# Performance work log

Measured on AMD Instinct MI355X. Metric: run time of the kernel, lower is better.

The kernel has to match this reference:

```python
import jax, jax.numpy as jnp
import numpy as np

N = 8192
F_IN = 128
OC1 = 64
OC2 = 64
N_CLASS = 16
AVG_DEG = 32.0


def setup_inputs() -> dict:
    key = jax.random.key(0)
    ks = jax.random.split(key, 10)
    # sparse-ish 0/1 adjacency with guaranteed self-loops (every row nonempty)
    A = (jax.random.uniform(ks[0], (N, N)) < (AVG_DEG / N)).astype(jnp.float32)
    A = jnp.maximum(A, jnp.eye(N, dtype=jnp.float32))
    deg = jnp.sum(A, axis=1)                      # [N]
    D = jnp.diag(deg)                             # diagonal degree matrix [N,N]
    X = jax.random.normal(ks[1], (N, F_IN), dtype=jnp.float32)
    s = 0.05
    W1 = jax.random.normal(ks[2], (F_IN, OC1), dtype=jnp.float32) * s
    b1 = jax.random.normal(ks[3], (OC1,), dtype=jnp.float32) * s
    W2 = jax.random.normal(ks[4], (OC1, OC2), dtype=jnp.float32) * s
    b2 = jax.random.normal(ks[5], (OC2,), dtype=jnp.float32) * s
    W3 = jax.random.normal(ks[6], (OC2, N_CLASS), dtype=jnp.float32) * s
    b3 = jax.random.normal(ks[7], (N_CLASS,), dtype=jnp.float32) * s
    return {"D": D, "X": X, "A": A, "W1": W1, "b1": b1,
            "W2": W2, "b2": b2, "W3": W3, "b3": b3}


def reference(D, X, A, W1, b1, W2, b2, W3, b3):
    # per-node degree: max over each row of the diagonal degree matrix
    deg = jnp.max(D, axis=1)                      # [N]
    # dj[0] in the original = degree of the FIRST (lowest-index) neighbor of i
    first_idx = jnp.argmax(A > 0, axis=1)         # [N]
    deg_first = deg[first_idx]                    # [N]
    # w[i,j] = A[i,j] / sqrt(deg_first[i] * deg[j]); zero where A[i,j]==0
    W = A / jnp.sqrt(deg_first[:, None] * deg[None, :])  # [N,N]

    def conv(H, Wl, bl):
        agg = W @ H                               # normalized neighbor aggregation
        return jax.nn.leaky_relu(agg @ Wl + bl)   # Linear + LeakyReLU(0.01)

    H = conv(X, W1, b1)
    # F.dropout in eval mode = identity
    H = conv(H, W2, b2)
    logits = H @ W3 + b3                          # [N, class_num]
    return jax.nn.log_softmax(logits, axis=1)
```

## Files before the change

kernel.cpp:

```cpp
#include <hip/hip_runtime.h>

#define NN   8192
#define FIN  128
#define CAP  128

typedef unsigned int u32x4 __attribute__((ext_vector_type(4)));

__global__ __launch_bounds__(256) void k_scan(
        const float* __restrict__ A,
        int* __restrict__ deg,
        int* __restrict__ first,
        unsigned short* __restrict__ cols,
        float* __restrict__ rsd) {
    __shared__ int s_cols[CAP];
    __shared__ int s_cnt, s_min;

    const int row = blockIdx.x;
    const int t   = threadIdx.x;
    if (t == 0) { s_cnt = 0; s_min = 0x7fffffff; }
    __syncthreads();

    const u32x4* Arow = (const u32x4*)(A + (size_t)row * NN);
    int lmin = 0x7fffffff;
#pragma unroll
    for (int v = 0; v < 8; ++v) {
        const int chunk = t + 256 * v;
        u32x4 q = __builtin_nontemporal_load(Arow + chunk);
        if (q.x | q.y | q.z | q.w) {
            unsigned int w[4] = {q.x, q.y, q.z, q.w};
#pragma unroll
            for (int h = 0; h < 4; ++h) {
                if (w[h]) {
                    int c = chunk * 4 + h;
                    int p = atomicAdd(&s_cnt, 1);
                    if (p < CAP) s_cols[p] = c;
                    lmin = min(lmin, c);
                }
            }
        }
    }
    if (lmin != 0x7fffffff) atomicMin(&s_min, lmin);
    __syncthreads();

    const int n = min(s_cnt, CAP);
    if (t < n) cols[row * CAP + t] = (unsigned short)s_cols[t];
    if (t == 0) {
        deg[row]   = s_cnt;
        first[row] = s_min;
        rsd[row]   = 1.0f / sqrtf((float)s_cnt);
    }
}

__global__ __launch_bounds__(128) void k_agg1(
        const float* __restrict__ X,
        const float* __restrict__ rsd,
        const float* __restrict__ W1,
        const float* __restrict__ b1,
        const int* __restrict__ deg,
        const int* __restrict__ first,
        const unsigned short* __restrict__ cols,
        float* __restrict__ H1) {
    __shared__ unsigned short s_cols[CAP];
    __shared__ float s_rsd[CAP];
    __shared__ float s_part[4][FIN];
    __shared__ float s_agg[FIN];
    __shared__ float s_lin[2][64];

    const int row = blockIdx.x;
    const int t   = threadIdx.x;
    const int n   = min(deg[row], CAP);

    if (t < n) {
        int c = cols[row * CAP + t];
        s_cols[t] = (unsigned short)c;
        s_rsd[t]  = rsd[c];
    }
    __syncthreads();

    {
        const int g = t >> 5, q = t & 31;
        const float4* X4 = (const float4*)X;
        float4 acc = make_float4(0.f, 0.f, 0.f, 0.f);
        for (int k = g; k < n; k += 4) {
            const float4 x = X4[(size_t)s_cols[k] * 32 + q];
            const float  r = s_rsd[k];
            acc.x += r * x.x; acc.y += r * x.y; acc.z += r * x.z; acc.w += r * x.w;
        }
        ((float4*)s_part[g])[q] = acc;
    }
    __syncthreads();

    const float alpha = rsd[first[row]];
    s_agg[t] = alpha * (s_part[0][t] + s_part[1][t] + s_part[2][t] + s_part[3][t]);
    __syncthreads();

    {
        const int c = t & 63, h = t >> 6;
        const int f0 = h * 64;
        float acc = h ? 0.f : b1[c];
#pragma unroll 8
        for (int f = 0; f < 64; ++f)
            acc += s_agg[f0 + f] * W1[(f0 + f) * 64 + c];
        s_lin[h][c] = acc;
    }
    __syncthreads();
    if (t < 64) {
        float a = s_lin[0][t] + s_lin[1][t];
        H1[(size_t)row * 64 + t] = a > 0.f ? a : 0.01f * a;
    }
}

__global__ __launch_bounds__(128) void k_agg2(
        const float* __restrict__ H1,
        const float* __restrict__ rsd,
        const float* __restrict__ W2,
        const float* __restrict__ b2,
        const float* __restrict__ W3,
        const float* __restrict__ b3,
        const int* __restrict__ deg,
        const int* __restrict__ first,
        const unsigned short* __restrict__ cols,
        float* __restrict__ out) {
    __shared__ unsigned short s_cols[CAP];
    __shared__ float s_rsd[CAP];
    __shared__ float s_part[8][64];
    __shared__ float s_agg[64];
    __shared__ float s_lin[2][64];
    __shared__ float s_h2[64];
    __shared__ float s_logit[16];

    const int row = blockIdx.x;
    const int t   = threadIdx.x;
    const int n   = min(deg[row], CAP);

    if (t < n) {
        int c = cols[row * CAP + t];
        s_cols[t] = (unsigned short)c;
        s_rsd[t]  = rsd[c];
    }
    __syncthreads();

    {
        const int g = t >> 4, q = t & 15;
        const float4* H4 = (const float4*)H1;
        float4 acc = make_float4(0.f, 0.f, 0.f, 0.f);
        for (int k = g; k < n; k += 8) {
            const float4 x = H4[(size_t)s_cols[k] * 16 + q];
            const float  r = s_rsd[k];
            acc.x += r * x.x; acc.y += r * x.y; acc.z += r * x.z; acc.w += r * x.w;
        }
        ((float4*)s_part[g])[q] = acc;
    }
    __syncthreads();

    const float alpha = rsd[first[row]];
    if (t < 64) {
        float s = 0.f;
#pragma unroll
        for (int g = 0; g < 8; ++g) s += s_part[g][t];
        s_agg[t] = alpha * s;
    }
    __syncthreads();

    {
        const int c = t & 63, h = t >> 6;
        const int f0 = h * 32;
        float acc = h ? 0.f : b2[c];
#pragma unroll
        for (int f = 0; f < 32; ++f)
            acc += s_agg[f0 + f] * W2[(f0 + f) * 64 + c];
        s_lin[h][c] = acc;
    }
    __syncthreads();
    if (t < 64) {
        float a = s_lin[0][t] + s_lin[1][t];
        s_h2[t] = a > 0.f ? a : 0.01f * a;
    }
    __syncthreads();

    if (t < 64) {
        const int c = t & 15, h = t >> 4;
        const int f0 = h * 16;
        float acc = h ? 0.f : b3[c];
#pragma unroll
        for (int f = 0; f < 16; ++f)
            acc += s_h2[f0 + f] * W3[(f0 + f) * 16 + c];
        s_part[h][c] = acc;
    }
    __syncthreads();
    if (t < 16)
        s_logit[t] = s_part[0][t] + s_part[1][t] + s_part[2][t] + s_part[3][t];
    __syncthreads();

    if (t < 16) {
        float m = -1e30f;
#pragma unroll
        for (int k = 0; k < 16; ++k) m = fmaxf(m, s_logit[k]);
        float s = 0.f;
#pragma unroll
        for (int k = 0; k < 16; ++k) s += expf(s_logit[k] - m);
        out[row * 16 + t] = s_logit[t] - m - logf(s);
    }
}

extern "C" void kernel_launch(void* const* d_in, const int* in_sizes, int n_in,
                              void* d_out, int out_size, void* d_ws, size_t ws_size,
                              hipStream_t stream) {
    const float* X  = (const float*)d_in[1];
    const float* A  = (const float*)d_in[2];
    const float* W1 = (const float*)d_in[3];
    const float* b1 = (const float*)d_in[4];
    const float* W2 = (const float*)d_in[5];
    const float* b2 = (const float*)d_in[6];
    const float* W3 = (const float*)d_in[7];
    const float* b3 = (const float*)d_in[8];

    char* ws = (char*)d_ws;
    float*          rsd   = (float*)(ws);
    int*            deg   = (int*)  (ws + 32768);
    int*            first = (int*)  (ws + 65536);
    float*          H1    = (float*)(ws + 98304);
    unsigned short* cols  = (unsigned short*)(ws + 98304 + 2097152);

    k_scan<<<NN, 256, 0, stream>>>(A, deg, first, cols, rsd);
    k_agg1<<<NN, 128, 0, stream>>>(X, rsd, W1, b1, deg, first, cols, H1);
    k_agg2<<<NN, 128, 0, stream>>>(H1, rsd, W2, b2, W3, b3, deg, first, cols,
                                   (float*)d_out);
}
```

Baseline: 479.8 us.

## Fuse scan and two aggregation stages into one persistent kernel with grid barriers

Replaces three launches with a single persistent kernel of 512 blocks, each owning 16 rows. Neighbor column lists stay in shared memory across phases, and global atomic grid barriers separate the phases. The aim is to cut launch overhead and the global round-trip of the cols/deg/first arrays. The gather loops are also unrolled by two for more memory-level parallelism. The cost is that the A scan, which dominates at 256MB read, now runs on only 512 blocks, which may reduce the bandwidth it achieves. The spin barrier also relies on all blocks being co-resident.

```diff
diff --git a/kernel.cpp b/kernel.cpp
--- a/kernel.cpp
+++ b/kernel.cpp
@@ -1,205 +1,229 @@
 #include <hip/hip_runtime.h>
 
-#define NN   8192
-#define FIN  128
-#define CAP  128
+#define NN    8192
+#define FIN   128
+#define CAP   128
+#define NBLK  512
+#define TPB   256
+#define RPB   16
 
 typedef unsigned int u32x4 __attribute__((ext_vector_type(4)));
 
-__global__ __launch_bounds__(256) void k_scan(
+__device__ __forceinline__ void grid_barrier(unsigned* ctr) {
+    __syncthreads();
+    if (threadIdx.x == 0) {
+        __threadfence();
+        __hip_atomic_fetch_add(ctr, 1u, __ATOMIC_ACQ_REL, __HIP_MEMORY_SCOPE_AGENT);
+        while (__hip_atomic_load(ctr, __ATOMIC_ACQUIRE, __HIP_MEMORY_SCOPE_AGENT)
+               < (unsigned)NBLK)
+            __builtin_amdgcn_s_sleep(2);
+        __threadfence();
+    }
+    __syncthreads();
+}
+
+__global__ __launch_bounds__(TPB, 2) void k_fused(
         const float* __restrict__ A,
-        int* __restrict__ deg,
-        int* __restrict__ first,
-        unsigned short* __restrict__ cols,
-        float* __restrict__ rsd) {
-    __shared__ int s_cols[CAP];
-    __shared__ int s_cnt, s_min;
-
-    const int row = blockIdx.x;
-    const int t   = threadIdx.x;
-    if (t == 0) { s_cnt = 0; s_min = 0x7fffffff; }
-    __syncthreads();
-
-    const u32x4* Arow = (const u32x4*)(A + (size_t)row * NN);
-    int lmin = 0x7fffffff;
-#pragma unroll
-    for (int v = 0; v < 8; ++v) {
-        const int chunk = t + 256 * v;
-        u32x4 q = __builtin_nontemporal_load(Arow + chunk);
-        if (q.x | q.y | q.z | q.w) {
-            unsigned int w[4] = {q.x, q.y, q.z, q.w};
-#pragma unroll
-            for (int h = 0; h < 4; ++h) {
-                if (w[h]) {
-                    int c = chunk * 4 + h;
-                    int p = atomicAdd(&s_cnt, 1);
-                    if (p < CAP) s_cols[p] = c;
-                    lmin = min(lmin, c);
-                }
-            }
-        }
-    }
-    if (lmin != 0x7fffffff) atomicMin(&s_min, lmin);
-    __syncthreads();
-
-    const int n = min(s_cnt, CAP);
-    if (t < n) cols[row * CAP + t] = (unsigned short)s_cols[t];
-    if (t == 0) {
-        deg[row]   = s_cnt;
-        first[row] = s_min;
-        rsd[row]   = 1.0f / sqrtf((float)s_cnt);
-    }
-}
-
-__global__ __launch_bounds__(128) void k_agg1(
         const float* __restrict__ X,
-        const float* __restrict__ rsd,
-        const float* __restrict__ W1,
-        const float* __restrict__ b1,
-        const int* __restrict__ deg,
-        const int* __restrict__ first,
-        const unsigned short* __restrict__ cols,
-        float* __restrict__ H1) {
-    __shared__ unsigned short s_cols[CAP];
+        const float* __restrict__ W1, const float* __restrict__ b1,
+        const float* __restrict__ W2, const float* __restrict__ b2,
+        const float* __restrict__ W3, const float* __restrict__ b3,
+        float* __restrict__ rsd,
+        float* __restrict__ H1,
+        unsigned* __restrict__ barrier_ctrs,
+        float* __restrict__ out) {
+    __shared__ unsigned short s_cols[RPB][CAP];
+    __shared__ int   s_deg[RPB];
+    __shared__ int   s_first[RPB];
     __shared__ float s_rsd[CAP];
-    __shared__ float s_part[4][FIN];
+    __shared__ float s_part[16][64];
     __shared__ float s_agg[FIN];
-    __shared__ float s_lin[2][64];
-
-    const int row = blockIdx.x;
-    const int t   = threadIdx.x;
-    const int n   = min(deg[row], CAP);
-
-    if (t < n) {
-        int c = cols[row * CAP + t];
-        s_cols[t] = (unsigned short)c;
-        s_rsd[t]  = rsd[c];
-    }
-    __syncthreads();
-
-    {
-        const int g = t >> 5, q = t & 31;
-        const float4* X4 = (const float4*)X;
-        float4 acc = make_float4(0.f, 0.f, 0.f, 0.f);
-        for (int k = g; k < n; k += 4) {
-            const float4 x = X4[(size_t)s_cols[k] * 32 + q];
-            const float  r = s_rsd[k];
-            acc.x += r * x.x; acc.y += r * x.y; acc.z += r * x.z; acc.w += r * x.w;
-        }
-        ((float4*)s_part[g])[q] = acc;
-    }
-    __syncthreads();
-
-    const float alpha = rsd[first[row]];
-    s_agg[t] = alpha * (s_part[0][t] + s_part[1][t] + s_part[2][t] + s_part[3][t]);
-    __syncthreads();
-
-    {
-        const int c = t & 63, h = t >> 6;
-        const int f0 = h * 64;
-        float acc = h ? 0.f : b1[c];
-#pragma unroll 8
-        for (int f = 0; f < 64; ++f)
-            acc += s_agg[f0 + f] * W1[(f0 + f) * 64 + c];
-        s_lin[h][c] = acc;
-    }
-    __syncthreads();
-    if (t < 64) {
-        float a = s_lin[0][t] + s_lin[1][t];
-        H1[(size_t)row * 64 + t] = a > 0.f ? a : 0.01f * a;
-    }
-}
-
-__global__ __launch_bounds__(128) void k_agg2(
-        const float* __restrict__ H1,
-        const float* __restrict__ rsd,
-        const float* __restrict__ W2,
-        const float* __restrict__ b2,
-        const float* __restrict__ W3,
-        const float* __restrict__ b3,
-        const int* __restrict__ deg,
-        const int* __restrict__ first,
-        const unsigned short* __restrict__ cols,
-        float* __restrict__ out) {
-    __shared__ unsigned short s_cols[CAP];
-    __shared__ float s_rsd[CAP];
-    __shared__ float s_part[8][64];
-    __shared__ float s_agg[64];
-    __shared__ float s_lin[2][64];
+    __shared__ float s_lin[4][64];
     __shared__ float s_h2[64];
     __shared__ float s_logit[16];
-
-    const int row = blockIdx.x;
-    const int t   = threadIdx.x;
-    const int n   = min(deg[row], CAP);
-
-    if (t < n) {
-        int c = cols[row * CAP + t];
-        s_cols[t] = (unsigned short)c;
-        s_rsd[t]  = rsd[c];
-    }
-    __syncthreads();
-
-    {
-        const int g = t >> 4, q = t & 15;
-        const float4* H4 = (const float4*)H1;
-        float4 acc = make_float4(0.f, 0.f, 0.f, 0.f);
-        for (int k = g; k < n; k += 8) {
-            const float4 x = H4[(size_t)s_cols[k] * 16 + q];
-            const float  r = s_rsd[k];
-            acc.x += r * x.x; acc.y += r * x.y; acc.z += r * x.z; acc.w += r * x.w;
-        }
-        ((float4*)s_part[g])[q] = acc;
-    }
-    __syncthreads();
-
-    const float alpha = rsd[first[row]];
-    if (t < 64) {
-        float s = 0.f;
-#pragma unroll
-        for (int g = 0; g < 8; ++g) s += s_part[g][t];
-        s_agg[t] = alpha * s;
-    }
-    __syncthreads();
-
-    {
-        const int c = t & 63, h = t >> 6;
-        const int f0 = h * 32;
-        float acc = h ? 0.f : b2[c];
-#pragma unroll
-        for (int f = 0; f < 32; ++f)
-            acc += s_agg[f0 + f] * W2[(f0 + f) * 64 + c];
-        s_lin[h][c] = acc;
-    }
-    __syncthreads();
-    if (t < 64) {
-        float a = s_lin[0][t] + s_lin[1][t];
-        s_h2[t] = a > 0.f ? a : 0.01f * a;
-    }
-    __syncthreads();
-
-    if (t < 64) {
-        const int c = t & 15, h = t >> 4;
-        const int f0 = h * 16;
-        float acc = h ? 0.f : b3[c];
-#pragma unroll
-        for (int f = 0; f < 16; ++f)
-            acc += s_h2[f0 + f] * W3[(f0 + f) * 16 + c];
-        s_part[h][c] = acc;
-    }
-    __syncthreads();
-    if (t < 16)
-        s_logit[t] = s_part[0][t] + s_part[1][t] + s_part[2][t] + s_part[3][t];
-    __syncthreads();
-
-    if (t < 16) {
-        float m = -1e30f;
-#pragma unroll
-        for (int k = 0; k < 16; ++k) m = fmaxf(m, s_logit[k]);
-        float s = 0.f;
-#pragma unroll
-        for (int k = 0; k < 16; ++k) s += expf(s_logit[k] - m);
-        out[row * 16 + t] = s_logit[t] - m - logf(s);
+    __shared__ int   s_cnt, s_min;
+
+    const int t = threadIdx.x;
+    const int b = blockIdx.x;
+
+    for (int r = 0; r < RPB; ++r) {
+        const int row = b * RPB + r;
+        if (t == 0) { s_cnt = 0; s_min = 0x7fffffff; }
+        __syncthreads();
+
+        const u32x4* Arow = (const u32x4*)(A + (size_t)row * NN);
+        int lmin = 0x7fffffff;
+#pragma unroll
+        for (int v = 0; v < 8; ++v) {
+            const int chunk = t + TPB * v;
+            u32x4 q = __builtin_nontemporal_load(Arow + chunk);
+            if (q.x | q.y | q.z | q.w) {
+                unsigned int w[4] = {q.x, q.y, q.z, q.w};
+#pragma unroll
+                for (int h = 0; h < 4; ++h) {
+                    if (w[h]) {
+                        int c = chunk * 4 + h;
+                        int p = atomicAdd(&s_cnt, 1);
+                        if (p < CAP) s_cols[r][p] = (unsigned short)c;
+                        lmin = min(lmin, c);
+                    }
+                }
+            }
+        }
+        if (lmin != 0x7fffffff) atomicMin(&s_min, lmin);
+        __syncthreads();
+        if (t == 0) {
+            int cnt = s_cnt;
+            s_deg[r]   = min(cnt, CAP);
+            s_first[r] = s_min;
+            rsd[row]   = 1.0f / sqrtf((float)cnt);
+        }
+        __syncthreads();
+    }
+
+    grid_barrier(&barrier_ctrs[0]);
+
+    for (int r = 0; r < RPB; ++r) {
+        const int row = b * RPB + r;
+        const int n   = s_deg[r];
+        if (t < n) s_rsd[t] = rsd[s_cols[r][t]];
+        __syncthreads();
+
+        {
+            const int g = t >> 5, q = t & 31;
+            const float4* X4 = (const float4*)X;
+            float4 acc = make_float4(0.f, 0.f, 0.f, 0.f);
+            int k = g;
+            while (k + 8 < n) {
+                const int c0 = s_cols[r][k], c1 = s_cols[r][k + 8];
+                const float4 x0 = X4[(size_t)c0 * 32 + q];
+                const float4 x1 = X4[(size_t)c1 * 32 + q];
+                const float r0 = s_rsd[k], r1 = s_rsd[k + 8];
+                acc.x += r0 * x0.x + r1 * x1.x;
+                acc.y += r0 * x0.y + r1 * x1.y;
+                acc.z += r0 * x0.z + r1 * x1.z;
+                acc.w += r0 * x0.w + r1 * x1.w;
+                k += 16;
+            }
+            if (k < n) {
+                const float4 x = X4[(size_t)s_cols[r][k] * 32 + q];
+                const float rr = s_rsd[k];
+                acc.x += rr * x.x; acc.y += rr * x.y;
+                acc.z += rr * x.z; acc.w += rr * x.w;
+            }
+            ((float4*)(&s_part[0][0] + g * FIN))[q] = acc;
+        }
+        __syncthreads();
+
+        const float alpha = rsd[s_first[r]];
+        if (t < FIN) {
+            float ssum = 0.f;
+#pragma unroll
+            for (int g = 0; g < 8; ++g) ssum += (&s_part[0][0])[g * FIN + t];
+            s_agg[t] = alpha * ssum;
+        }
+        __syncthreads();
+
+        {
+            const int c = t & 63, h = t >> 6;
+            const int f0 = h * 32;
+            float acc = h ? 0.f : b1[c];
+#pragma unroll
+            for (int f = 0; f < 32; ++f)
+                acc += s_agg[f0 + f] * W1[(f0 + f) * 64 + c];
+            s_lin[h][c] = acc;
+        }
+        __syncthreads();
+        if (t < 64) {
+            float a = s_lin[0][t] + s_lin[1][t] + s_lin[2][t] + s_lin[3][t];
+            H1[(size_t)row * 64 + t] = a > 0.f ? a : 0.01f * a;
+        }
+        __syncthreads();
+    }
+
+    grid_barrier(&barrier_ctrs[1]);
+
+    for (int r = 0; r < RPB; ++r) {
+        const int row = b * RPB + r;
+        const int n   = s_deg[r];
+        if (t < n) s_rsd[t] = rsd[s_cols[r][t]];
+        __syncthreads();
+
+        {
+            const int g = t >> 4, q = t & 15;
+            const float4* H4 = (const float4*)H1;
+            float4 acc = make_float4(0.f, 0.f, 0.f, 0.f);
+            int k = g;
+            while (k + 16 < n) {
+                const int c0 = s_cols[r][k], c1 = s_cols[r][k + 16];
+                const float4 x0 = H4[(size_t)c0 * 16 + q];
+                const float4 x1 = H4[(size_t)c1 * 16 + q];
+                const float r0 = s_rsd[k], r1 = s_rsd[k + 16];
+                acc.x += r0 * x0.x + r1 * x1.x;
+                acc.y += r0 * x0.y + r1 * x1.y;
+                acc.z += r0 * x0.z + r1 * x1.z;
+                acc.w += r0 * x0.w + r1 * x1.w;
+                k += 32;
+            }
+            if (k < n) {
+                const float4 x = H4[(size_t)s_cols[r][k] * 16 + q];
+                const float rr = s_rsd[k];
+                acc.x += rr * x.x; acc.y += rr * x.y;
+                acc.z += rr * x.z; acc.w += rr * x.w;
+            }
+            ((float4*)s_part[g])[q] = acc;
+        }
+        __syncthreads();
+
+        const float alpha = rsd[s_first[r]];
+        if (t < 64) {
+            float ssum = 0.f;
+#pragma unroll
+            for (int g = 0; g < 16; ++g) ssum += s_part[g][t];
+            s_agg[t] = alpha * ssum;
+        }
+        __syncthreads();
+
+        {
+            const int c = t & 63, h = t >> 6;
+            const int f0 = h * 16;
+            float acc = h ? 0.f : b2[c];
+#pragma unroll
+            for (int f = 0; f < 16; ++f)
+                acc += s_agg[f0 + f] * W2[(f0 + f) * 64 + c];
+            s_lin[h][c] = acc;
+        }
+        __syncthreads();
+        if (t < 64) {
+            float a = s_lin[0][t] + s_lin[1][t] + s_lin[2][t] + s_lin[3][t];
+            s_h2[t] = a > 0.f ? a : 0.01f * a;
+        }
+        __syncthreads();
+
+        if (t < 64) {
+            const int c = t & 15, h = t >> 4;
+            const int f0 = h * 16;
+            float acc = h ? 0.f : b3[c];
+#pragma unroll
+            for (int f = 0; f < 16; ++f)
+                acc += s_h2[f0 + f] * W3[(f0 + f) * 16 + c];
+            s_lin[h][c] = acc;
+        }
+        __syncthreads();
+        if (t < 16)
+            s_logit[t] = s_lin[0][t] + s_lin[1][t] + s_lin[2][t] + s_lin[3][t];
+        __syncthreads();
+
+        if (t < 16) {
+            float m = -1e30f;
+#pragma unroll
+            for (int k = 0; k < 16; ++k) m = fmaxf(m, s_logit[k]);
+            float s = 0.f;
+#pragma unroll
+            for (int k = 0; k < 16; ++k) s += expf(s_logit[k] - m);
+            out[row * 16 + t] = s_logit[t] - m - logf(s);
+        }
+        __syncthreads();
     }
 }
 
@@ -214,16 +238,15 @@
     const float* b2 = (const float*)d_in[6];
     const float* W3 = (const float*)d_in[7];
     const float* b3 = (const float*)d_in[8];
+    float* out = (float*)d_out;
 
     char* ws = (char*)d_ws;
-    float*          rsd   = (float*)(ws);
-    int*            deg   = (int*)  (ws + 32768);
-    int*            first = (int*)  (ws + 65536);
-    float*          H1    = (float*)(ws + 98304);
-    unsigned short* cols  = (unsigned short*)(ws + 98304 + 2097152);
-
-    k_scan<<<NN, 256, 0, stream>>>(A, deg, first, cols, rsd);
-    k_agg1<<<NN, 128, 0, stream>>>(X, rsd, W1, b1, deg, first, cols, H1);
-    k_agg2<<<NN, 128, 0, stream>>>(H1, rsd, W2, b2, W3, b3, deg, first, cols,
-                                   (float*)d_out);
+    float*    rsd  = (float*)(ws);
+    float*    H1   = (float*)(ws + 32768);
+    unsigned* ctrs = (unsigned*)(ws + 32768 + 2097152);
+
+    hipMemsetAsync(ctrs, 0, 2 * sizeof(unsigned), stream);
+
+    k_fused<<<NBLK, TPB, 0, stream>>>(A, X, W1, b1, W2, b2, W3, b3,
+                                      rsd, H1, ctrs, out);
 }
```

New measurement: 713.1 us. +48.6%, slower.

## Double aggregation block size, unroll neighbor gather by two, drop nontemporal A loads

Applied to the files above, without the earlier changes.

Both aggregation kernels now launch 256 threads per row instead of 128, splitting the neighbor gather across twice as many groups and the linear layer across four feature slices. The gather loop handles two neighbors per iteration, putting more independent loads in flight. The alpha load is hoisted ahead of the first barrier. The scan of the dense adjacency switches from nontemporal to ordinary loads. The added threads bring more shared-memory partial sums to reduce, and the load change may alter cache behaviour on the large A stream, which dominates runtime.

```diff
diff --git a/kernel.cpp b/kernel.cpp
--- a/kernel.cpp
+++ b/kernel.cpp
@@ -25,7 +25,7 @@
 #pragma unroll
     for (int v = 0; v < 8; ++v) {
         const int chunk = t + 256 * v;
-        u32x4 q = __builtin_nontemporal_load(Arow + chunk);
+        u32x4 q = Arow[chunk];
         if (q.x | q.y | q.z | q.w) {
             unsigned int w[4] = {q.x, q.y, q.z, q.w};
 #pragma unroll
@@ -51,7 +51,7 @@
     }
 }
 
-__global__ __launch_bounds__(128) void k_agg1(
+__global__ __launch_bounds__(256) void k_agg1(
         const float* __restrict__ X,
         const float* __restrict__ rsd,
         const float* __restrict__ W1,
@@ -62,13 +62,14 @@
         float* __restrict__ H1) {
     __shared__ unsigned short s_cols[CAP];
     __shared__ float s_rsd[CAP];
-    __shared__ float s_part[4][FIN];
+    __shared__ float s_part[8][FIN];
     __shared__ float s_agg[FIN];
-    __shared__ float s_lin[2][64];
+    __shared__ float s_lin[4][64];
 
     const int row = blockIdx.x;
     const int t   = threadIdx.x;
     const int n   = min(deg[row], CAP);
+    const float alpha = rsd[first[row]];
 
     if (t < n) {
         int c = cols[row * CAP + t];
@@ -81,36 +82,53 @@
         const int g = t >> 5, q = t & 31;
         const float4* X4 = (const float4*)X;
         float4 acc = make_float4(0.f, 0.f, 0.f, 0.f);
-        for (int k = g; k < n; k += 4) {
+        int k = g;
+        while (k + 8 < n) {
+            const int c0 = s_cols[k], c1 = s_cols[k + 8];
+            const float4 x0 = X4[(size_t)c0 * 32 + q];
+            const float4 x1 = X4[(size_t)c1 * 32 + q];
+            const float r0 = s_rsd[k], r1 = s_rsd[k + 8];
+            acc.x += r0 * x0.x + r1 * x1.x;
+            acc.y += r0 * x0.y + r1 * x1.y;
+            acc.z += r0 * x0.z + r1 * x1.z;
+            acc.w += r0 * x0.w + r1 * x1.w;
+            k += 16;
+        }
+        if (k < n) {
             const float4 x = X4[(size_t)s_cols[k] * 32 + q];
-            const float  r = s_rsd[k];
-            acc.x += r * x.x; acc.y += r * x.y; acc.z += r * x.z; acc.w += r * x.w;
+            const float rr = s_rsd[k];
+            acc.x += rr * x.x; acc.y += rr * x.y;
+            acc.z += rr * x.z; acc.w += rr * x.w;
         }
         ((float4*)s_part[g])[q] = acc;
     }
     __syncthreads();
 
-    const float alpha = rsd[first[row]];
-    s_agg[t] = alpha * (s_part[0][t] + s_part[1][t] + s_part[2][t] + s_part[3][t]);
+    if (t < FIN) {
+        float ssum = 0.f;
+#pragma unroll
+        for (int g = 0; g < 8; ++g) ssum += s_part[g][t];
+        s_agg[t] = alpha * ssum;
+    }
     __syncthreads();
 
     {
         const int c = t & 63, h = t >> 6;
-        const int f0 = h * 64;
+        const int f0 = h * 32;
         float acc = h ? 0.f : b1[c];
-#pragma unroll 8
-        for (int f = 0; f < 64; ++f)
+#pragma unroll
+        for (int f = 0; f < 32; ++f)
             acc += s_agg[f0 + f] * W1[(f0 + f) * 64 + c];
         s_lin[h][c] = acc;
     }
     __syncthreads();
     if (t < 64) {
-        float a = s_lin[0][t] + s_lin[1][t];
+        float a = s_lin[0][t] + s_lin[1][t] + s_lin[2][t] + s_lin[3][t];
         H1[(size_t)row * 64 + t] = a > 0.f ? a : 0.01f * a;
     }
 }
 
-__global__ __launch_bounds__(128) void k_agg2(
+__global__ __launch_bounds__(256) void k_agg2(
         const float* __restrict__ H1,
         const float* __restrict__ rsd,
         const float* __restrict__ W2,
@@ -123,15 +141,16 @@
         float* __restrict__ out) {
     __shared__ unsigned short s_cols[CAP];
     __shared__ float s_rsd[CAP];
-    __shared__ float s_part[8][64];
+    __shared__ float s_part[16][64];
     __shared__ float s_agg[64];
-    __shared__ float s_lin[2][64];
+    __shared__ float s_lin[4][64];
     __shared__ float s_h2[64];
     __shared__ float s_logit[16];
 
     const int row = blockIdx.x;
     const int t   = threadIdx.x;
     const int n   = min(deg[row], CAP);
+    const float alpha = rsd[first[row]];
 
     if (t < n) {
         int c = cols[row * CAP + t];
@@ -144,36 +163,48 @@
         const int g = t >> 4, q = t & 15;
         const float4* H4 = (const float4*)H1;
         float4 acc = make_float4(0.f, 0.f, 0.f, 0.f);
-        for (int k = g; k < n; k += 8) {
+        int k = g;
+        while (k + 16 < n) {
+            const int c0 = s_cols[k], c1 = s_cols[k + 16];
+            const float4 x0 = H4[(size_t)c0 * 16 + q];
+            const float4 x1 = H4[(size_t)c1 * 16 + q];
+            const float r0 = s_rsd[k], r1 = s_rsd[k + 16];
+            acc.x += r0 * x0.x + r1 * x1.x;
+            acc.y += r0 * x0.y + r1 * x1.y;
+            acc.z += r0 * x0.z + r1 * x1.z;
+            acc.w += r0 * x0.w + r1 * x1.w;
+            k += 32;
+        }
+        if (k < n) {
             const float4 x = H4[(size_t)s_cols[k] * 16 + q];
-            const float  r = s_rsd[k];
-            acc.x += r * x.x; acc.y += r * x.y; acc.z += r * x.z; acc.w += r * x.w;
+            const float rr = s_rsd[k];
+            acc.x += rr * x.x; acc.y += rr * x.y;
+            acc.z += rr * x.z; acc.w += rr * x.w;
         }
         ((float4*)s_part[g])[q] = acc;
     }
     __syncthreads();
 
-    const float alpha = rsd[first[row]];
-    if (t < 64) {
-        float s = 0.f;
-#pragma unroll
-        for (int g = 0; g < 8; ++g) s += s_part[g][t];
-        s_agg[t] = alpha * s;
+    if (t < 64) {
+        float ssum = 0.f;
+#pragma unroll
+        for (int g = 0; g < 16; ++g) ssum += s_part[g][t];
+        s_agg[t] = alpha * ssum;
     }
     __syncthreads();
 
     {
         const int c = t & 63, h = t >> 6;
-        const int f0 = h * 32;
+        const int f0 = h * 16;
         float acc = h ? 0.f : b2[c];
 #pragma unroll
-        for (int f = 0; f < 32; ++f)
+        for (int f = 0; f < 16; ++f)
             acc += s_agg[f0 + f] * W2[(f0 + f) * 64 + c];
         s_lin[h][c] = acc;
     }
     __syncthreads();
     if (t < 64) {
-        float a = s_lin[0][t] + s_lin[1][t];
+        float a = s_lin[0][t] + s_lin[1][t] + s_lin[2][t] + s_lin[3][t];
         s_h2[t] = a > 0.f ? a : 0.01f * a;
     }
     __syncthreads();
@@ -185,11 +216,11 @@
 #pragma unroll
         for (int f = 0; f < 16; ++f)
             acc += s_h2[f0 + f] * W3[(f0 + f) * 16 + c];
-        s_part[h][c] = acc;
+        s_lin[h][c] = acc;
     }
     __syncthreads();
     if (t < 16)
-        s_logit[t] = s_part[0][t] + s_part[1][t] + s_part[2][t] + s_part[3][t];
+        s_logit[t] = s_lin[0][t] + s_lin[1][t] + s_lin[2][t] + s_lin[3][t];
     __syncthreads();
 
     if (t < 16) {
@@ -223,7 +254,7 @@
     unsigned short* cols  = (unsigned short*)(ws + 98304 + 2097152);
 
     k_scan<<<NN, 256, 0, stream>>>(A, deg, first, cols, rsd);
-    k_agg1<<<NN, 128, 0, stream>>>(X, rsd, W1, b1, deg, first, cols, H1);
-    k_agg2<<<NN, 128, 0, stream>>>(H1, rsd, W2, b2, W3, b3, deg, first, cols,
+    k_agg1<<<NN, 256, 0, stream>>>(X, rsd, W1, b1, deg, first, cols, H1);
+    k_agg2<<<NN, 256, 0, stream>>>(H1, rsd, W2, b2, W3, b3, deg, first, cols,
                                    (float*)d_out);
 }
```

New measurement: 502.4 us. 1.05x slower.
